# Kernel tuning notes

Hardware: AMD Instinct MI355X
Metric: run time of the kernel (lower is better)

The kernel has to match this reference:

```python
import jax, jax.numpy as jnp
import numpy as np
import math

EMBED_DIM = 128
NUM_HEADS = 8
HEAD_DIM = EMBED_DIM // NUM_HEADS
# Faithful to the source's concat bug: heads [0,1,1,2,3,4,5,6] (head 7 dropped, head 1 duplicated)
HEAD_ORDER = [0, 1, 1, 2, 3, 4, 5, 6]


def setup_inputs() -> dict:
    key = jax.random.key(0)
    ks = jax.random.split(key, 7)
    B, S = 4, 2048
    input_embeddings = jax.random.normal(ks[0], (B, S, EMBED_DIM), dtype=jnp.float32)
    token_attention_masks = jax.random.randint(ks[1], (B, S), 0, 2, dtype=jnp.int64)
    # torch.rand -> uniform [0,1)
    w_query = jax.random.uniform(ks[2], (EMBED_DIM, EMBED_DIM), dtype=jnp.float32)
    w_key = jax.random.uniform(ks[3], (EMBED_DIM, EMBED_DIM), dtype=jnp.float32)
    w_value = jax.random.uniform(ks[4], (EMBED_DIM, EMBED_DIM), dtype=jnp.float32)
    # nn.Linear params
    lim = 1.0 / math.sqrt(EMBED_DIM)
    lin_w = jax.random.uniform(ks[5], (EMBED_DIM, EMBED_DIM), dtype=jnp.float32, minval=-lim, maxval=lim)
    lin_b = jax.random.uniform(ks[6], (EMBED_DIM,), dtype=jnp.float32, minval=-lim, maxval=lim)
    return {"input_embeddings": input_embeddings, "token_attention_masks": token_attention_masks,
            "w_query": w_query, "w_key": w_key, "w_value": w_value, "lin_w": lin_w, "lin_b": lin_b}


def reference(input_embeddings, token_attention_masks, w_query, w_key, w_value, lin_w, lin_b):
    B, S, _ = input_embeddings.shape
    q = input_embeddings @ w_query  # [B,S,D]
    k = input_embeddings @ w_key
    v = input_embeddings @ w_value
    # split heads: [B,S,H,hd] -> [B,H,S,hd]
    qh = q.reshape(B, S, NUM_HEADS, HEAD_DIM).transpose(0, 2, 1, 3)
    kh = k.reshape(B, S, NUM_HEADS, HEAD_DIM).transpose(0, 2, 1, 3)
    vh = v.reshape(B, S, NUM_HEADS, HEAD_DIM).transpose(0, 2, 1, 3)
    # NOTE: source scales by sqrt(full embedding dim), not sqrt(head_dim)
    scale = 1.0 / math.sqrt(EMBED_DIM)
    scores = jnp.einsum('bhsd,bhtd->bhst', qh, kh) * scale  # [B,H,S,S]
    # mask: 0 -> -1000, 1 -> 0; broadcast over query positions
    mask = jnp.where(token_attention_masks == 0, -1000.0, 0.0).astype(scores.dtype)  # [B,S]
    scores = scores + mask[:, None, None, :]
    probs = jax.nn.softmax(scores, axis=-1)
    out_h = jnp.einsum('bhst,bhtd->bhsd', probs, vh)  # [B,H,S,hd]
    # buggy concat order kept faithful
    attn_out = jnp.concatenate([out_h[:, i] for i in HEAD_ORDER], axis=-1)  # [B,S,D]
    return attn_out @ lin_w.T + lin_b
```

## Files before the change

kernel.cpp:

```cpp
#include <hip/hip_runtime.h>
#include <stdint.h>

typedef unsigned short u16;
typedef unsigned int   u32;
typedef int     i32x4  __attribute__((ext_vector_type(4)));
typedef float   f32x4  __attribute__((ext_vector_type(4)));
typedef float   f32x16 __attribute__((ext_vector_type(16)));
typedef __bf16  bf16x8 __attribute__((ext_vector_type(8)));
typedef u32     u32x4  __attribute__((ext_vector_type(4)));
typedef u32     u32x2  __attribute__((ext_vector_type(2)));

union BF8 { bf16x8 v; u16 s[8]; u32x4 q; };

__device__ __forceinline__ u16 f2b_rne(float f) {
    u32 u = __builtin_bit_cast(u32, f);
    u32 r = u + 0x7FFFu + ((u >> 16) & 1u);
    return (u16)(r >> 16);
}
__device__ __forceinline__ u16 f2b_trunc(float f) {
    return (u16)(__builtin_bit_cast(u32, f) >> 16);
}
__device__ __forceinline__ float b2f(u16 h) {
    u32 u = ((u32)h) << 16;
    return __builtin_bit_cast(float, u);
}
__device__ __forceinline__ bf16x8 ld_bf8(const u16* p) {
    BF8 t; t.q = *(const u32x4*)p; return t.v;
}
__device__ __forceinline__ f32x16 zero16() {
    f32x16 z;
#pragma unroll
    for (int i = 0; i < 16; i++) z[i] = 0.f;
    return z;
}
__device__ __forceinline__ f32x4 zero4() {
    f32x4 z;
#pragma unroll
    for (int i = 0; i < 4; i++) z[i] = 0.f;
    return z;
}

#define SCALE2 0.1275312959479341f

__device__ __forceinline__ void st_ao(u16* aob, int row, int col, u16 v) {
    int blk = (col >> 3) ^ (row & 15);
    aob[row * 128 + blk * 8 + (col & 7)] = v;
}

__global__ __launch_bounds__(256) void proj_kernel(
    const float* __restrict__ x, const float* __restrict__ wq,
    const float* __restrict__ wk, const float* __restrict__ wv,
    const int* __restrict__ mask, int* __restrict__ Larr,
    u16* Qph, u16* Qpl, u16* Kph, u16* Kpl, u16* VT)
{
    int typ  = blockIdx.y;
    int ct   = threadIdx.x >> 6;
    int lane = threadIdx.x & 63;
    int m = lane & 31, kg = lane >> 5;
    int r0 = blockIdx.x * 32;
    int c = ct * 32 + m;
    int b = r0 >> 11, sl = r0 & 2047;

    __shared__ int pos_sh[32];
    __shared__ int Lsh;

    if (typ != 0) {
        if (threadIdx.x < 64) {
            int tl = threadIdx.x;
            const int* mp = mask + b * 2048 + tl * 32;
            int mv[32]; int cntv = 0;
#pragma unroll
            for (int j4 = 0; j4 < 8; j4++) {
                i32x4 t = *(const i32x4*)(mp + j4 * 4);
#pragma unroll
                for (int q = 0; q < 4; q++) {
                    mv[j4 * 4 + q] = t[q];
                    cntv += (t[q] != 0);
                }
            }
            int off = cntv;
#pragma unroll
            for (int d = 1; d < 64; d <<= 1) {
                int o = __shfl_up(off, d, 64);
                if (tl >= d) off += o;
            }
            if (tl == 63) Lsh = off;
            if (tl == (sl >> 5)) {
                int p = off - cntv;
#pragma unroll
                for (int j = 0; j < 32; j++) {
                    pos_sh[j] = mv[j] ? p : -1;
                    p += (mv[j] != 0);
                }
            }
        }
        __syncthreads();
    }

    const float* wp = (typ == 0) ? wq : (typ == 1) ? wk : wv;

    f32x16 acc = zero16();
#pragma unroll 4
    for (int kk = 0; kk < 128; kk += 16) {
        const float* xp = x + (size_t)(r0 + m) * 128 + kk + kg * 8;
        f32x4 x0 = *(const f32x4*)xp;
        f32x4 x1 = *(const f32x4*)(xp + 4);
        BF8 ah, al;
#pragma unroll
        for (int j = 0; j < 4; j++) {
            u16 hb = f2b_trunc(x0[j]);
            ah.s[j] = hb; al.s[j] = f2b_trunc(x0[j] - b2f(hb));
            u16 hb2 = f2b_trunc(x1[j]);
            ah.s[4 + j] = hb2; al.s[4 + j] = f2b_trunc(x1[j] - b2f(hb2));
        }
        const float* wcol = wp + (size_t)(kk + kg * 8) * 128 + c;
        if (typ < 2) {
            BF8 bh, bl_;
#pragma unroll
            for (int j = 0; j < 8; j++) {
                float w = wcol[(size_t)j * 128];
                u16 hb = f2b_trunc(w);
                bh.s[j] = hb; bl_.s[j] = f2b_trunc(w - b2f(hb));
            }
            acc = __builtin_amdgcn_mfma_f32_32x32x16_bf16(ah.v, bh.v, acc, 0, 0, 0);
            acc = __builtin_amdgcn_mfma_f32_32x32x16_bf16(ah.v, bl_.v, acc, 0, 0, 0);
            acc = __builtin_amdgcn_mfma_f32_32x32x16_bf16(al.v, bh.v, acc, 0, 0, 0);
        } else {
            BF8 bh;
#pragma unroll
            for (int j = 0; j < 8; j++) bh.s[j] = f2b_rne(wcol[(size_t)j * 128]);
            acc = __builtin_amdgcn_mfma_f32_32x32x16_bf16(ah.v, bh.v, acc, 0, 0, 0);
        }
    }

    int hh = c >> 4, d = c & 15;
    if (typ == 0) {
        if (hh == 7) return;
        size_t hb_off = (size_t)(b * 8 + hh) * 2048 * 16 + d;
#pragma unroll
        for (int r = 0; r < 16; r++) {
            int row = (r & 3) + 8 * (r >> 2) + 4 * kg;
            float v = acc[r] * SCALE2;
            u16 hi = f2b_trunc(v);
            size_t idx = hb_off + (size_t)(sl + row) * 16;
            Qph[idx] = hi;
            Qpl[idx] = f2b_trunc(v - b2f(hi));
        }
    } else if (typ == 1) {
        if (hh == 7) return;
        size_t hb_off = (size_t)(b * 8 + hh) * 2048 * 16 + d;
#pragma unroll
        for (int r = 0; r < 16; r++) {
            int row = (r & 3) + 8 * (r >> 2) + 4 * kg;
            int p = pos_sh[row];
            if (p < 0) continue;
            float v = acc[r];
            u16 hi = f2b_trunc(v);
            size_t idx = hb_off + (size_t)p * 16;
            Kph[idx] = hi;
            Kpl[idx] = f2b_trunc(v - b2f(hi));
        }
    } else {
        if (hh != 7) {
#pragma unroll
            for (int rg = 0; rg < 4; rg++) {
#pragma unroll
                for (int q = 0; q < 4; q++) {
                    int row = rg * 8 + 4 * kg + q;
                    int p = pos_sh[row];
                    if (p >= 0)
                        VT[(size_t)(b * 128 + c) * 2048 + p] = f2b_rne(acc[rg * 4 + q]);
                }
            }
        }
        int L = Lsh;
        int npad = (L + 127) & ~127; if (npad < 128) npad = 128;
        int padn = npad - L;
        int slice = blockIdx.x & 63;
        if (padn > 0) {
            int e = slice * 256 + threadIdx.x;
            int k = e & 127, cc = e >> 7;
            if (k < padn) VT[(size_t)(b * 128 + cc) * 2048 + (L + k)] = 0;
        }
        if (slice == 0 && threadIdx.x == 0) Larr[b] = L;
    }
}

__global__ __launch_bounds__(448, 2) void attn_kernel(
    const u16* __restrict__ Qph, const u16* __restrict__ Qpl,
    const u16* __restrict__ Kph, const u16* __restrict__ Kpl,
    const u16* __restrict__ VT, const int* __restrict__ Larr,
    const float* __restrict__ lw, const float* __restrict__ lb,
    float* __restrict__ out)
{
    __shared__ char smem[23552];
    u16*   pbuf = (u16*)smem;
    u16*   aob  = (u16*)(smem + 14336);
    float* sclb = (float*)(smem + 22528);

    int bid = blockIdx.x;
    int b = bid >> 6, qt = bid & 63;
    int wave = threadIdx.x >> 6;
    int lane = threadIdx.x & 63;
    int m = lane & 31, kg = lane >> 5;
    int qs = qt * 32;
    int h = wave;

    int L = Larr[b];
    int npad = (L + 127) & ~127; if (npad < 128) npad = 128;

    size_t headoff = (size_t)(b * 8 + h) * 2048 * 16;
    bf16x8 qfh = ld_bf8(Qph + headoff + (size_t)(qs + m) * 16 + kg * 8);
    bf16x8 qfl = ld_bf8(Qpl + headoff + (size_t)(qs + m) * 16 + kg * 8);
    const u16* kbh = Kph + headoff;
    const u16* kbl = Kpl + headoff;

    f32x4 o0 = zero4(), o1 = zero4(), l0 = zero4(), l1 = zero4();
    float m_run = -3.0e38f;
    BF8 onesu;
#pragma unroll
    for (int j = 0; j < 8; j++) onesu.s[j] = 0x3F80;
    bf16x8 ones = onesu.v;

    int q16 = lane & 15, krow = lane >> 4;
    const u16* vtb = VT + (size_t)(b * 128 + h * 16 + q16) * 2048;
    int msw = (m >> 1) & 3;
    int qsw = (q16 >> 1) & 3;
    u16* pwb = pbuf + wave * 1024 + m * 32 + kg * 4;
    const u16* pr0 = pbuf + wave * 1024 + q16 * 32 + ((krow ^ qsw) * 8);
    const u16* pr1 = pr0 + 16 * 32;
    float* scl = sclb + wave * 32;

    bf16x8 khc = ld_bf8(kbh + (size_t)m * 16 + kg * 8);
    bf16x8 klc = ld_bf8(kbl + (size_t)m * 16 + kg * 8);

    for (int t = 0; t < npad; t += 32) {
        int tn = (t + 32 < npad) ? (t + 32) : 0;
        bf16x8 khn = ld_bf8(kbh + (size_t)(tn + m) * 16 + kg * 8);
        bf16x8 kln = ld_bf8(kbl + (size_t)(tn + m) * 16 + kg * 8);
        bf16x8 vf  = ld_bf8(vtb + t + krow * 8);

        f32x16 sc = zero16();
        sc = __builtin_amdgcn_mfma_f32_32x32x16_bf16(khc, qfl, sc, 0, 0, 0);
        sc = __builtin_amdgcn_mfma_f32_32x32x16_bf16(klc, qfh, sc, 0, 0, 0);
        sc = __builtin_amdgcn_mfma_f32_32x32x16_bf16(khc, qfh, sc, 0, 0, 0);
        bool tail = (t + 32 > L);

        float tmax = -3.0e38f;
        if (!tail) {
#pragma unroll
            for (int r = 0; r < 16; r++) tmax = fmaxf(tmax, sc[r]);
        } else {
#pragma unroll
            for (int r = 0; r < 16; r++) {
                int key = t + (r & 3) + 8 * (r >> 2) + 4 * kg;
                if (key < L) tmax = fmaxf(tmax, sc[r]);
            }
        }
        tmax = fmaxf(tmax, __shfl_xor(tmax, 32, 64));

        if (__any(tmax > m_run + 8.0f)) {
            float mnew = fmaxf(m_run, tmax);
            float s = __builtin_amdgcn_exp2f(m_run - mnew);
            if (kg == 0) scl[m] = s;
            m_run = mnew;
            f32x4 s0 = *(const f32x4*)(scl + krow * 4);
            f32x4 s1 = *(const f32x4*)(scl + krow * 4 + 16);
#pragma unroll
            for (int j = 0; j < 4; j++) {
                o0[j] *= s0[j]; l0[j] *= s0[j];
                o1[j] *= s1[j]; l1[j] *= s1[j];
            }
        }

#pragma unroll
        for (int rg = 0; rg < 4; rg++) {
            float e0 = __builtin_amdgcn_exp2f(sc[rg * 4 + 0] - m_run);
            float e1 = __builtin_amdgcn_exp2f(sc[rg * 4 + 1] - m_run);
            float e2 = __builtin_amdgcn_exp2f(sc[rg * 4 + 2] - m_run);
            float e3 = __builtin_amdgcn_exp2f(sc[rg * 4 + 3] - m_run);
            if (tail) {
                int kb = t + rg * 8 + kg * 4;
                e0 = (kb + 0 < L) ? e0 : 0.f;
                e1 = (kb + 1 < L) ? e1 : 0.f;
                e2 = (kb + 2 < L) ? e2 : 0.f;
                e3 = (kb + 3 < L) ? e3 : 0.f;
            }
            u32x2 pk;
            pk[0] = __builtin_amdgcn_perm(__builtin_bit_cast(u32, e1),
                                          __builtin_bit_cast(u32, e0), 0x07060302u);
            pk[1] = __builtin_amdgcn_perm(__builtin_bit_cast(u32, e3),
                                          __builtin_bit_cast(u32, e2), 0x07060302u);
            *(u32x2*)(pwb + ((rg ^ msw) * 8)) = pk;
        }
        bf16x8 p0 = *(const bf16x8*)pr0;
        bf16x8 p1 = *(const bf16x8*)pr1;
        o0 = __builtin_amdgcn_mfma_f32_16x16x32_bf16(p0, vf, o0, 0, 0, 0);
        o1 = __builtin_amdgcn_mfma_f32_16x16x32_bf16(p1, vf, o1, 0, 0, 0);
        l0 = __builtin_amdgcn_mfma_f32_16x16x32_bf16(p0, ones, l0, 0, 0, 0);
        l1 = __builtin_amdgcn_mfma_f32_16x16x32_bf16(p1, ones, l1, 0, 0, 0);
        khc = khn; klc = kln;
    }

    int slot0 = (h == 0) ? 0 : h + 1;
#pragma unroll
    for (int j = 0; j < 4; j++) {
        int row0 = krow * 4 + j;
        u16 v0 = f2b_rne(o0[j] * __builtin_amdgcn_rcpf(l0[j]));
        u16 v1 = f2b_rne(o1[j] * __builtin_amdgcn_rcpf(l1[j]));
        int col = slot0 * 16 + q16;
        st_ao(aob, row0,      col, v0);
        st_ao(aob, row0 + 16, col, v1);
        if (h == 1) {
            st_ao(aob, row0,      16 + q16, v0);
            st_ao(aob, row0 + 16, 16 + q16, v1);
        }
    }

    __syncthreads();
    if (threadIdx.x >= 256) return;

    int ct2 = threadIdx.x >> 6;
    int c = ct2 * 32 + m;
    int r0 = b * 2048 + qs;
    f32x16 acc = zero16();
#pragma unroll 4
    for (int kk = 0; kk < 128; kk += 16) {
        int col0 = kk + kg * 8;
        int blk = (col0 >> 3) ^ (m & 15);
        bf16x8 af = *(const bf16x8*)(aob + m * 128 + blk * 8);
        const float* wp2 = lw + (size_t)c * 128 + col0;
        f32x4 w0 = *(const f32x4*)wp2;
        f32x4 w1 = *(const f32x4*)(wp2 + 4);
        BF8 bfr;
#pragma unroll
        for (int j = 0; j < 4; j++) {
            bfr.s[j]     = f2b_rne(w0[j]);
            bfr.s[4 + j] = f2b_rne(w1[j]);
        }
        acc = __builtin_amdgcn_mfma_f32_32x32x16_bf16(af, bfr.v, acc, 0, 0, 0);
    }
    float bias = lb[c];
#pragma unroll
    for (int r = 0; r < 16; r++) {
        int row = (r & 3) + 8 * (r >> 2) + 4 * kg;
        out[(size_t)(r0 + row) * 128 + c] = acc[r] + bias;
    }
}

extern "C" void kernel_launch(void* const* d_in, const int* in_sizes, int n_in,
                              void* d_out, int out_size, void* d_ws, size_t ws_size,
                              hipStream_t stream)
{
    const float* x    = (const float*)d_in[0];
    const int*   mask = (const int*)d_in[1];
    const float* wq   = (const float*)d_in[2];
    const float* wk   = (const float*)d_in[3];
    const float* wv   = (const float*)d_in[4];
    const float* lw   = (const float*)d_in[5];
    const float* lb   = (const float*)d_in[6];
    float* out = (float*)d_out;

    char* ws = (char*)d_ws;
    u16* Qph = (u16*)(ws + 0 * 2097152);
    u16* Qpl = (u16*)(ws + 1 * 2097152);
    u16* Kph = (u16*)(ws + 2 * 2097152);
    u16* Kpl = (u16*)(ws + 3 * 2097152);
    u16* VT  = (u16*)(ws + 4 * 2097152);
    int* Larr = (int*)(ws + 5 * 2097152);

    proj_kernel<<<dim3(256, 3), 256, 0, stream>>>(x, wq, wk, wv, mask, Larr,
                                                  Qph, Qpl, Kph, Kpl, VT);
    attn_kernel<<<256, 448, 0, stream>>>(Qph, Qpl, Kph, Kpl, VT, Larr,
                                         lw, lb, out);
}
```

Before: 107.5 us.

## Software-pipeline QK score MFMAs one tile ahead of softmax and PV

Computes the next tile's QK^T scores (three bf16 split-precision MFMAs) before the current tile's PV MFMAs, so the score matrix for iteration t+1 is in flight while softmax and PV for tile t run. The V fragment is also prefetched one tile ahead. The row max is changed from a serial fmax chain to a tree reduction to shorten the dependency chain. This costs extra registers for a second 16-float score accumulator and prefetched V, which can lower occupancy, and it adds one redundant score computation on the wrap-around tile.

```diff
diff --git a/kernel.cpp b/kernel.cpp
--- a/kernel.cpp
+++ b/kernel.cpp
@@ -45,6 +45,16 @@
 __device__ __forceinline__ void st_ao(u16* aob, int row, int col, u16 v) {
     int blk = (col >> 3) ^ (row & 15);
     aob[row * 128 + blk * 8 + (col & 7)] = v;
+}
+
+__device__ __forceinline__ float max16(const float* v) {
+    float a0 = fmaxf(v[0], v[1]),  a1 = fmaxf(v[2], v[3]);
+    float a2 = fmaxf(v[4], v[5]),  a3 = fmaxf(v[6], v[7]);
+    float a4 = fmaxf(v[8], v[9]),  a5 = fmaxf(v[10], v[11]);
+    float a6 = fmaxf(v[12], v[13]), a7 = fmaxf(v[14], v[15]);
+    float b0 = fmaxf(a0, a1), b1 = fmaxf(a2, a3);
+    float b2 = fmaxf(a4, a5), b3 = fmaxf(a6, a7);
+    return fmaxf(fmaxf(b0, b1), fmaxf(b2, b3));
 }
 
 __global__ __launch_bounds__(256) void proj_kernel(
@@ -233,29 +243,34 @@
 
     bf16x8 khc = ld_bf8(kbh + (size_t)m * 16 + kg * 8);
     bf16x8 klc = ld_bf8(kbl + (size_t)m * 16 + kg * 8);
+    bf16x8 vfc = ld_bf8(vtb + krow * 8);
+    f32x16 sc_c = zero16();
+    sc_c = __builtin_amdgcn_mfma_f32_32x32x16_bf16(khc, qfl, sc_c, 0, 0, 0);
+    sc_c = __builtin_amdgcn_mfma_f32_32x32x16_bf16(klc, qfh, sc_c, 0, 0, 0);
+    sc_c = __builtin_amdgcn_mfma_f32_32x32x16_bf16(khc, qfh, sc_c, 0, 0, 0);
 
     for (int t = 0; t < npad; t += 32) {
         int tn = (t + 32 < npad) ? (t + 32) : 0;
         bf16x8 khn = ld_bf8(kbh + (size_t)(tn + m) * 16 + kg * 8);
         bf16x8 kln = ld_bf8(kbl + (size_t)(tn + m) * 16 + kg * 8);
-        bf16x8 vf  = ld_bf8(vtb + t + krow * 8);
-
-        f32x16 sc = zero16();
-        sc = __builtin_amdgcn_mfma_f32_32x32x16_bf16(khc, qfl, sc, 0, 0, 0);
-        sc = __builtin_amdgcn_mfma_f32_32x32x16_bf16(klc, qfh, sc, 0, 0, 0);
-        sc = __builtin_amdgcn_mfma_f32_32x32x16_bf16(khc, qfh, sc, 0, 0, 0);
+        bf16x8 vfn = ld_bf8(vtb + tn + krow * 8);
+
         bool tail = (t + 32 > L);
 
-        float tmax = -3.0e38f;
+        float tmax;
         if (!tail) {
-#pragma unroll
-            for (int r = 0; r < 16; r++) tmax = fmaxf(tmax, sc[r]);
+            float tv[16];
+#pragma unroll
+            for (int r = 0; r < 16; r++) tv[r] = sc_c[r];
+            tmax = max16(tv);
         } else {
+            float tv[16];
 #pragma unroll
             for (int r = 0; r < 16; r++) {
                 int key = t + (r & 3) + 8 * (r >> 2) + 4 * kg;
-                if (key < L) tmax = fmaxf(tmax, sc[r]);
-            }
+                tv[r] = (key < L) ? sc_c[r] : -3.0e38f;
+            }
+            tmax = max16(tv);
         }
         tmax = fmaxf(tmax, __shfl_xor(tmax, 32, 64));
 
@@ -275,10 +290,10 @@
 
 #pragma unroll
         for (int rg = 0; rg < 4; rg++) {
-            float e0 = __builtin_amdgcn_exp2f(sc[rg * 4 + 0] - m_run);
-            float e1 = __builtin_amdgcn_exp2f(sc[rg * 4 + 1] - m_run);
-            float e2 = __builtin_amdgcn_exp2f(sc[rg * 4 + 2] - m_run);
-            float e3 = __builtin_amdgcn_exp2f(sc[rg * 4 + 3] - m_run);
+            float e0 = __builtin_amdgcn_exp2f(sc_c[rg * 4 + 0] - m_run);
+            float e1 = __builtin_amdgcn_exp2f(sc_c[rg * 4 + 1] - m_run);
+            float e2 = __builtin_amdgcn_exp2f(sc_c[rg * 4 + 2] - m_run);
+            float e3 = __builtin_amdgcn_exp2f(sc_c[rg * 4 + 3] - m_run);
             if (tail) {
                 int kb = t + rg * 8 + kg * 4;
                 e0 = (kb + 0 < L) ? e0 : 0.f;
@@ -295,11 +310,18 @@
         }
         bf16x8 p0 = *(const bf16x8*)pr0;
         bf16x8 p1 = *(const bf16x8*)pr1;
-        o0 = __builtin_amdgcn_mfma_f32_16x16x32_bf16(p0, vf, o0, 0, 0, 0);
-        o1 = __builtin_amdgcn_mfma_f32_16x16x32_bf16(p1, vf, o1, 0, 0, 0);
+
+        f32x16 sc_n = zero16();
+        sc_n = __builtin_amdgcn_mfma_f32_32x32x16_bf16(khn, qfl, sc_n, 0, 0, 0);
+        sc_n = __builtin_amdgcn_mfma_f32_32x32x16_bf16(kln, qfh, sc_n, 0, 0, 0);
+        sc_n = __builtin_amdgcn_mfma_f32_32x32x16_bf16(khn, qfh, sc_n, 0, 0, 0);
+
+        o0 = __builtin_amdgcn_mfma_f32_16x16x32_bf16(p0, vfc, o0, 0, 0, 0);
+        o1 = __builtin_amdgcn_mfma_f32_16x16x32_bf16(p1, vfc, o1, 0, 0, 0);
         l0 = __builtin_amdgcn_mfma_f32_16x16x32_bf16(p0, ones, l0, 0, 0, 0);
         l1 = __builtin_amdgcn_mfma_f32_16x16x32_bf16(p1, ones, l1, 0, 0, 0);
-        khc = khn; klc = kln;
+
+        sc_c = sc_n; vfc = vfn;
     }
 
     int slot0 = (h == 0) ? 0 : h + 1;
```

Result: no change. 109.0 us (+1.4%).
